# Optimization experiments

Hardware: AMD Instinct MI355X
Metric: run time of the kernel (lower is better)

## Reference

```python
import jax, jax.numpy as jnp
import numpy as np

N = 100000      # nodes
E = 3200000     # edges (avg degree 32)
IN, HID, OUT = 512, 256, 64
K = 10
ALPHA = 0.1


def setup_inputs() -> dict:
    key = jax.random.key(0)
    k1, k2, k3, k4 = jax.random.split(key, 4)
    x = jax.random.normal(k1, (N, IN), dtype=jnp.float32)
    edge_index = jax.random.randint(k2, (2, E), 0, N, dtype=jnp.int64)
    # MLP params (Kaiming-ish scaling)
    W1 = jax.random.normal(k3, (IN, HID), dtype=jnp.float32) / np.sqrt(IN)
    b1 = jnp.zeros((HID,), dtype=jnp.float32)
    W2 = jax.random.normal(k4, (HID, OUT), dtype=jnp.float32) / np.sqrt(HID)
    b2 = jnp.zeros((OUT,), dtype=jnp.float32)
    # GPR_prop PPR init: temp[k] = alpha*(1-alpha)^k, temp[K] = (1-alpha)^K
    ks = np.arange(K + 1)
    temp = ALPHA * (1.0 - ALPHA) ** ks
    temp[-1] = (1.0 - ALPHA) ** K
    temp = jnp.asarray(temp, dtype=jnp.float32)
    return {"x": x, "edge_index": edge_index, "W1": W1, "b1": b1,
            "W2": W2, "b2": b2, "temp": temp}


def reference(x, edge_index, W1, b1, W2, b2, temp):
    # MLP front-end (eval mode: dropout = identity)
    h = jax.nn.relu(x @ W1 + b1)
    h = h @ W2 + b2                                  # [N, OUT]

    # gcn_norm with self-loops: A_hat = D^{-1/2} (A + I) D^{-1/2}
    loop = jnp.arange(N, dtype=edge_index.dtype)
    src = jnp.concatenate([edge_index[0], loop])      # [E+N]
    dst = jnp.concatenate([edge_index[1], loop])      # [E+N]
    deg = jax.ops.segment_sum(jnp.ones_like(dst, dtype=h.dtype), dst,
                              num_segments=N)
    dis = jnp.where(deg > 0, jax.lax.rsqrt(deg), 0.0)
    norm = (dis[src] * dis[dst])[:, None]             # [E+N, 1]

    # GPR propagation: out = sum_k temp[k] * A_hat^k h
    def step(carry, gamma):
        hk, acc = carry
        hk = jax.ops.segment_sum(norm * hk[src], dst, num_segments=N)
        return (hk, acc + gamma * hk), None

    (_, out), _ = jax.lax.scan(step, (h, temp[0] * h), temp[1:])
    return out
```

## Files before the change

### kernel.cpp

```cpp
#include <hip/hip_runtime.h>

#define NN 100000
#define NE 3200000
#define DIN 512
#define DHID 256
#define DOUT 64
#define KPROP 10
#define NPART 8
#define PSZ 12500

typedef _Float16 f16;
typedef _Float16 f16x8 __attribute__((ext_vector_type(8)));
typedef _Float16 f16x4 __attribute__((ext_vector_type(4)));
typedef float f32x4 __attribute__((ext_vector_type(4)));

__global__ void detect_i64(const int* __restrict__ ei, int* __restrict__ flag) {
  int lane = threadIdx.x;
  int ok = 1;
  for (int i = lane; i < 512; i += 64)
    if (ei[2 * i + 1] != 0) ok = 0;
  ok = __all(ok);
  if (lane == 0) *flag = ok;
}

__global__ void zero_cnt(int* __restrict__ cnt) {
  int g = blockIdx.x * blockDim.x + threadIdx.x;
  if (g < NN) cnt[g] = 0;
}

__global__ __launch_bounds__(256) void count_deg(
    const int* __restrict__ ei, const int* __restrict__ flag,
    int* __restrict__ cnt) {
  int p = blockIdx.x & 7;
  int chunk = blockIdx.x >> 3;
  int e0 = chunk * 1024 + threadIdx.x * 4;
  if (e0 >= NE) return;
  int is64 = *flag;
  int d0, d1, d2, d3;
  if (is64) {
    int4 a = *(const int4*)&ei[2 * (size_t)NE + 2 * (size_t)e0];
    int4 b = *(const int4*)&ei[2 * (size_t)NE + 2 * (size_t)e0 + 4];
    d0 = a.x; d1 = a.z; d2 = b.x; d3 = b.z;
  } else {
    int4 a = *(const int4*)&ei[(size_t)NE + e0];
    d0 = a.x; d1 = a.y; d2 = a.z; d3 = a.w;
  }
  int lo = p * PSZ, hi = lo + PSZ;
  if (d0 >= lo && d0 < hi) atomicAdd(&cnt[d0], 1);
  if (d1 >= lo && d1 < hi) atomicAdd(&cnt[d1], 1);
  if (d2 >= lo && d2 < hi) atomicAdd(&cnt[d2], 1);
  if (d3 >= lo && d3 < hi) atomicAdd(&cnt[d3], 1);
}

__global__ void scan1(const int* __restrict__ cnt, int* __restrict__ rs,
                      int* __restrict__ bsum) {
  __shared__ int tmp[1024];
  int t = threadIdx.x;
  int g = blockIdx.x * 1024 + t;
  int v = (g < NN) ? cnt[g] : 0;
  tmp[t] = v;
  __syncthreads();
  for (int off = 1; off < 1024; off <<= 1) {
    int y = (t >= off) ? tmp[t - off] : 0;
    __syncthreads();
    tmp[t] += y;
    __syncthreads();
  }
  if (g < NN) rs[g] = tmp[t] - v;
  if (t == 1023) bsum[blockIdx.x] = tmp[t];
}

__global__ void scan2(int* __restrict__ bsum, int nb) {
  if (blockIdx.x == 0 && threadIdx.x == 0) {
    int s = 0;
    for (int i = 0; i < nb; i++) { int v = bsum[i]; bsum[i] = s; s += v; }
  }
}

__global__ void scan3_and_dis(int* __restrict__ rs, const int* __restrict__ bsum,
                              int* __restrict__ cursor, const int* __restrict__ cnt,
                              float* __restrict__ dis) {
  int g = blockIdx.x * blockDim.x + threadIdx.x;
  if (g < NN) {
    int v = rs[g] + bsum[g >> 10];
    rs[g] = v;
    cursor[g] = v;
    dis[g] = rsqrtf((float)(cnt[g] + 1));
  }
}

__global__ __launch_bounds__(256) void fill_csr(
    const int* __restrict__ ei, const int* __restrict__ flag,
    const float* __restrict__ dis, int* __restrict__ cursor,
    int2* __restrict__ recs) {
  int p = blockIdx.x & 7;
  int chunk = blockIdx.x >> 3;
  int e0 = chunk * 1024 + threadIdx.x * 4;
  if (e0 >= NE) return;
  int is64 = *flag;
  int d[4];
  if (is64) {
    int4 a = *(const int4*)&ei[2 * (size_t)NE + 2 * (size_t)e0];
    int4 b = *(const int4*)&ei[2 * (size_t)NE + 2 * (size_t)e0 + 4];
    d[0] = a.x; d[1] = a.z; d[2] = b.x; d[3] = b.z;
  } else {
    int4 a = *(const int4*)&ei[(size_t)NE + e0];
    d[0] = a.x; d[1] = a.y; d[2] = a.z; d[3] = a.w;
  }
  int lo = p * PSZ, hi = lo + PSZ;
  #pragma unroll
  for (int j = 0; j < 4; j++) {
    if (d[j] >= lo && d[j] < hi) {
      int s = is64 ? ei[2 * (size_t)(e0 + j)] : ei[e0 + j];
      int pos = atomicAdd(&cursor[d[j]], 1);
      recs[pos] = make_int2(s, __float_as_int(dis[s] * dis[d[j]]));
    }
  }
}

__global__ void cvt_weights(const float* __restrict__ W1, const float* __restrict__ W2,
                            f16* __restrict__ W1t, f16* __restrict__ W2t) {
  int g = blockIdx.x * 256 + threadIdx.x;
  if (g < DIN * DHID) {
    int k = g >> 8, n = g & 255;
    W1t[(size_t)n * DIN + k] = (f16)W1[g];
  }
  if (g < DHID * DOUT) {
    int k = g >> 6, n = g & 63;
    W2t[(size_t)n * DHID + k] = (f16)W2[g];
  }
}

__global__ __launch_bounds__(256) void mlp_mfma(
    const float* __restrict__ x, const f16* __restrict__ W1t,
    const float* __restrict__ b1, const f16* __restrict__ W2t,
    const float* __restrict__ b2, const float* __restrict__ temp,
    f16* __restrict__ h, f16* __restrict__ z)
{
  __shared__ __align__(16) char smraw[2 * 64 * 136 * 2];
  f16* xsb = (f16*)smraw;
  f16* h1s = (f16*)smraw;
  int t = threadIdx.x;
  int lane = t & 63;
  int w = t >> 6;
  int n0 = blockIdx.x * 64;
  int r15 = lane & 15;
  int g4 = lane >> 4;
  int nbase = w * 64;
  int srow = t >> 5, sc4 = t & 31;

  f32x4 acc[4][4];
  #pragma unroll
  for (int nt = 0; nt < 4; nt++) {
    float bv = b1[nbase + nt * 16 + r15];
    #pragma unroll
    for (int mt = 0; mt < 4; mt++) acc[mt][nt] = (f32x4){bv, bv, bv, bv};
  }

  float4 ld[8];
  #pragma unroll
  for (int it = 0; it < 8; it++) {
    int row = srow + it * 8;
    int gr = n0 + row;
    ld[it] = (gr < NN) ? *(const float4*)&x[(size_t)gr * DIN + sc4 * 4]
                       : make_float4(0.f, 0.f, 0.f, 0.f);
  }
  #pragma unroll
  for (int it = 0; it < 8; it++) {
    int row = srow + it * 8;
    f16x4 hv = { (f16)ld[it].x, (f16)ld[it].y, (f16)ld[it].z, (f16)ld[it].w };
    *(f16x4*)&xsb[row * 136 + sc4 * 4] = hv;
  }
  __syncthreads();

  for (int c = 0; c < 4; c++) {
    int cur = c & 1;
    if (c < 3) {
      #pragma unroll
      for (int it = 0; it < 8; it++) {
        int row = srow + it * 8;
        int gr = n0 + row;
        ld[it] = (gr < NN)
            ? *(const float4*)&x[(size_t)gr * DIN + (c + 1) * 128 + sc4 * 4]
            : make_float4(0.f, 0.f, 0.f, 0.f);
      }
    }
    int k0 = c * 128;
    const f16* xs = xsb + cur * 8704;
    #pragma unroll
    for (int ks = 0; ks < 4; ks++) {
      int kk = ks * 32 + g4 * 8;
      f16x8 a[4], b[4];
      #pragma unroll
      for (int mt = 0; mt < 4; mt++)
        a[mt] = *(const f16x8*)&xs[(mt * 16 + r15) * 136 + kk];
      #pragma unroll
      for (int nt = 0; nt < 4; nt++)
        b[nt] = *(const f16x8*)&W1t[(size_t)(nbase + nt * 16 + r15) * DIN + k0 + kk];
      #pragma unroll
      for (int mt = 0; mt < 4; mt++)
        #pragma unroll
        for (int nt = 0; nt < 4; nt++)
          acc[mt][nt] = __builtin_amdgcn_mfma_f32_16x16x32_f16(a[mt], b[nt], acc[mt][nt], 0, 0, 0);
    }
    if (c < 3) {
      #pragma unroll
      for (int it = 0; it < 8; it++) {
        int row = srow + it * 8;
        f16x4 hv = { (f16)ld[it].x, (f16)ld[it].y, (f16)ld[it].z, (f16)ld[it].w };
        *(f16x4*)&xsb[(cur ^ 1) * 8704 + row * 136 + sc4 * 4] = hv;
      }
    }
    __syncthreads();
  }

  #pragma unroll
  for (int mt = 0; mt < 4; mt++)
    #pragma unroll
    for (int nt = 0; nt < 4; nt++)
      #pragma unroll
      for (int r = 0; r < 4; r++) {
        float v = fmaxf(acc[mt][nt][r], 0.f);
        h1s[(mt * 16 + g4 * 4 + r) * 264 + nbase + nt * 16 + r15] = (f16)v;
      }
  __syncthreads();

  f32x4 acc2[4];
  #pragma unroll
  for (int nt = 0; nt < 4; nt++) {
    float bv = b2[nt * 16 + r15];
    acc2[nt] = (f32x4){bv, bv, bv, bv};
  }
  #pragma unroll
  for (int ks = 0; ks < 8; ks++) {
    int kk = ks * 32 + g4 * 8;
    f16x8 a2 = *(const f16x8*)&h1s[(w * 16 + r15) * 264 + kk];
    #pragma unroll
    for (int nt = 0; nt < 4; nt++) {
      f16x8 bf = *(const f16x8*)&W2t[(size_t)(nt * 16 + r15) * DHID + kk];
      acc2[nt] = __builtin_amdgcn_mfma_f32_16x16x32_f16(a2, bf, acc2[nt], 0, 0, 0);
    }
  }
  float tK = temp[KPROP];
  #pragma unroll
  for (int nt = 0; nt < 4; nt++)
    #pragma unroll
    for (int r = 0; r < 4; r++) {
      int node = n0 + w * 16 + g4 * 4 + r;
      if (node < NN) {
        int colv = nt * 16 + r15;
        float v = acc2[nt][r];
        h[(size_t)node * DOUT + colv] = (f16)v;
        z[(size_t)node * DOUT + colv] = (f16)(tK * v);
      }
    }
}

__global__ __launch_bounds__(256) void prop_horner(
    const f16* __restrict__ z, f16* __restrict__ zn, const f16* __restrict__ h,
    float* __restrict__ out, const int* __restrict__ rs, const int* __restrict__ cnt,
    const int2* __restrict__ recs, const float* __restrict__ dis,
    const float* __restrict__ temp, int kidx, int final_step)
{
  int w = blockIdx.x * 4 + (threadIdx.x >> 6);
  int lane = threadIdx.x & 63;
  if (w >= NN) return;
  int q = lane >> 3;
  int s8 = lane & 7;

  float acc[8];
  #pragma unroll
  for (int f = 0; f < 8; f++) acc[f] = 0.f;

  int beg = rs[w], n = cnt[w];
  const int2* rp = recs + beg;

  int e = 0;
  for (; e + 32 <= n; e += 32) {
    int2 r0 = rp[e + q];
    int2 r1 = rp[e + 8 + q];
    int2 r2 = rp[e + 16 + q];
    int2 r3 = rp[e + 24 + q];
    f16x8 g0 = *(const f16x8*)&z[(size_t)r0.x * DOUT + s8 * 8];
    f16x8 g1 = *(const f16x8*)&z[(size_t)r1.x * DOUT + s8 * 8];
    f16x8 g2 = *(const f16x8*)&z[(size_t)r2.x * DOUT + s8 * 8];
    f16x8 g3 = *(const f16x8*)&z[(size_t)r3.x * DOUT + s8 * 8];
    float w0 = __int_as_float(r0.y);
    float w1 = __int_as_float(r1.y);
    float w2 = __int_as_float(r2.y);
    float w3 = __int_as_float(r3.y);
    #pragma unroll
    for (int f = 0; f < 8; f++) acc[f] = fmaf(w0, (float)g0[f], acc[f]);
    #pragma unroll
    for (int f = 0; f < 8; f++) acc[f] = fmaf(w1, (float)g1[f], acc[f]);
    #pragma unroll
    for (int f = 0; f < 8; f++) acc[f] = fmaf(w2, (float)g2[f], acc[f]);
    #pragma unroll
    for (int f = 0; f < 8; f++) acc[f] = fmaf(w3, (float)g3[f], acc[f]);
  }
  for (; e + 8 <= n; e += 8) {
    int2 r0 = rp[e + q];
    f16x8 g0 = *(const f16x8*)&z[(size_t)r0.x * DOUT + s8 * 8];
    float w0 = __int_as_float(r0.y);
    #pragma unroll
    for (int f = 0; f < 8; f++) acc[f] = fmaf(w0, (float)g0[f], acc[f]);
  }
  if (e < n) {
    int rem = n - e;
    int qq = q < rem ? q : rem - 1;
    int2 r0 = rp[e + qq];
    f16x8 g0 = *(const f16x8*)&z[(size_t)r0.x * DOUT + s8 * 8];
    float w0 = (q < rem) ? __int_as_float(r0.y) : 0.f;
    #pragma unroll
    for (int f = 0; f < 8; f++) acc[f] = fmaf(w0, (float)g0[f], acc[f]);
  }

  #pragma unroll
  for (int f = 0; f < 8; f++) {
    acc[f] += __shfl_xor(acc[f], 8);
    acc[f] += __shfl_xor(acc[f], 16);
    acc[f] += __shfl_xor(acc[f], 32);
  }

  if (q == 0) {
    float dd = dis[w];
    float dd2 = dd * dd;
    float gk = temp[kidx];
    f16x8 zs = *(const f16x8*)&z[(size_t)w * DOUT + s8 * 8];
    f16x8 hs = *(const f16x8*)&h[(size_t)w * DOUT + s8 * 8];
    #pragma unroll
    for (int f = 0; f < 8; f++)
      acc[f] += dd2 * (float)zs[f] + gk * (float)hs[f];
    if (final_step) {
      float4 o0 = { acc[0], acc[1], acc[2], acc[3] };
      float4 o1 = { acc[4], acc[5], acc[6], acc[7] };
      *(float4*)&out[(size_t)w * DOUT + s8 * 8] = o0;
      *(float4*)&out[(size_t)w * DOUT + s8 * 8 + 4] = o1;
    } else {
      f16x8 o;
      #pragma unroll
      for (int f = 0; f < 8; f++) o[f] = (f16)acc[f];
      *(f16x8*)&zn[(size_t)w * DOUT + s8 * 8] = o;
    }
  }
}

extern "C" void kernel_launch(void* const* d_in, const int* in_sizes, int n_in,
                              void* d_out, int out_size, void* d_ws, size_t ws_size,
                              hipStream_t stream) {
  const float* x    = (const float*)d_in[0];
  const int*   ei   = (const int*)d_in[1];
  const float* W1   = (const float*)d_in[2];
  const float* b1   = (const float*)d_in[3];
  const float* W2   = (const float*)d_in[4];
  const float* b2   = (const float*)d_in[5];
  const float* temp = (const float*)d_in[6];
  float* out = (float*)d_out;

  char* wsb = (char*)d_ws;
  size_t off = 0;
  auto carve = [&](size_t bytes) -> void* {
    void* p = wsb + off;
    off = (off + bytes + 255) & ~(size_t)255;
    return p;
  };
  int*   cnt    = (int*)carve((size_t)NN * 4);
  int*   rs     = (int*)carve((size_t)NN * 4);
  int*   cursor = (int*)carve((size_t)NN * 4);
  int*   bsum   = (int*)carve(128 * 4);
  int*   flag   = (int*)carve(256);
  float* dis    = (float*)carve((size_t)NN * 4);
  int2*  recs   = (int2*)carve((size_t)NE * 8);
  f16*   W1t    = (f16*)carve((size_t)DHID * DIN * 2);
  f16*   W2t    = (f16*)carve((size_t)DOUT * DHID * 2);
  f16*   h_buf  = (f16*)carve((size_t)NN * DOUT * 2);
  f16*   z_a    = (f16*)carve((size_t)NN * DOUT * 2);
  f16*   z_b    = (f16*)carve((size_t)NN * DOUT * 2);
  if (off > ws_size) return;

  int nchunks = NE / 1024;

  detect_i64<<<1, 64, 0, stream>>>(ei, flag);
  zero_cnt<<<(NN + 255) / 256, 256, 0, stream>>>(cnt);
  count_deg<<<nchunks * NPART, 256, 0, stream>>>(ei, flag, cnt);
  scan1<<<(NN + 1023) / 1024, 1024, 0, stream>>>(cnt, rs, bsum);
  scan2<<<1, 64, 0, stream>>>(bsum, (NN + 1023) / 1024);
  scan3_and_dis<<<(NN + 255) / 256, 256, 0, stream>>>(rs, bsum, cursor, cnt, dis);
  fill_csr<<<nchunks * NPART, 256, 0, stream>>>(ei, flag, dis, cursor, recs);

  cvt_weights<<<(DIN * DHID + 255) / 256, 256, 0, stream>>>(W1, W2, W1t, W2t);
  mlp_mfma<<<(NN + 63) / 64, 256, 0, stream>>>(x, W1t, b1, W2t, b2, temp, h_buf, z_a);

  const f16* zc = z_a;
  f16* zn = z_b;
  for (int k = KPROP - 1; k >= 0; k--) {
    prop_horner<<<(NN + 3) / 4, 256, 0, stream>>>(zc, zn, h_buf, out, rs, cnt,
                                                  recs, dis, temp, k, k == 0);
    const f16* t2 = zn;
    zn = (f16*)zc;
    zc = t2;
  }
}
```

Measured before the change: 1.017 ms.

## Store features in 16-column blocks and propagate per feature block

The MLP now writes h and z in a column-blocked layout (four blocks of 16 features, each holding all nodes contiguously). Propagation launches separate block groups per feature block, with two threads per destination node each gathering 16 bytes. Each pass over a feature block only touches a 3.2 MB slice of z, which is meant to stay cache-resident and improve gather locality. In exchange, the edge records are read four times, each thread walks its edge list serially with no cross-lane reduction, and the 32-byte gathers per node are narrower than the previous 128-byte rows.

```diff
diff --git a/kernel.cpp b/kernel.cpp
--- a/kernel.cpp
+++ b/kernel.cpp
@@ -8,6 +8,7 @@
 #define KPROP 10
 #define NPART 8
 #define PSZ 12500
+#define NBLK 782
 
 typedef _Float16 f16;
 typedef _Float16 f16x8 __attribute__((ext_vector_type(8)));
@@ -135,7 +136,7 @@
     const float* __restrict__ x, const f16* __restrict__ W1t,
     const float* __restrict__ b1, const f16* __restrict__ W2t,
     const float* __restrict__ b2, const float* __restrict__ temp,
-    f16* __restrict__ h, f16* __restrict__ z)
+    f16* __restrict__ hcm, f16* __restrict__ zcm)
 {
   __shared__ __align__(16) char smraw[2 * 64 * 136 * 2];
   f16* xsb = (f16*)smraw;
@@ -248,100 +249,80 @@
     for (int r = 0; r < 4; r++) {
       int node = n0 + w * 16 + g4 * 4 + r;
       if (node < NN) {
-        int colv = nt * 16 + r15;
+        size_t o = (size_t)nt * NN * 16 + (size_t)node * 16 + r15;
         float v = acc2[nt][r];
-        h[(size_t)node * DOUT + colv] = (f16)v;
-        z[(size_t)node * DOUT + colv] = (f16)(tK * v);
+        hcm[o] = (f16)v;
+        zcm[o] = (f16)(tK * v);
       }
     }
 }
 
-__global__ __launch_bounds__(256) void prop_horner(
-    const f16* __restrict__ z, f16* __restrict__ zn, const f16* __restrict__ h,
+__global__ __launch_bounds__(256) void prop_fb(
+    const f16* __restrict__ z, f16* __restrict__ zn, const f16* __restrict__ hcm,
     float* __restrict__ out, const int* __restrict__ rs, const int* __restrict__ cnt,
     const int2* __restrict__ recs, const float* __restrict__ dis,
     const float* __restrict__ temp, int kidx, int final_step)
 {
-  int w = blockIdx.x * 4 + (threadIdx.x >> 6);
-  int lane = threadIdx.x & 63;
-  if (w >= NN) return;
-  int q = lane >> 3;
-  int s8 = lane & 7;
+  int fb = blockIdx.x / NBLK;
+  int nb = blockIdx.x - fb * NBLK;
+  int t = threadIdx.x;
+  int dst = nb * 128 + (t >> 1);
+  if (dst >= NN) return;
+  int p = t & 1;
+  const f16* zs = z + (size_t)fb * NN * 16 + p * 8;
 
   float acc[8];
   #pragma unroll
   for (int f = 0; f < 8; f++) acc[f] = 0.f;
 
-  int beg = rs[w], n = cnt[w];
+  int beg = rs[dst], n = cnt[dst];
   const int2* rp = recs + beg;
-
   int e = 0;
-  for (; e + 32 <= n; e += 32) {
-    int2 r0 = rp[e + q];
-    int2 r1 = rp[e + 8 + q];
-    int2 r2 = rp[e + 16 + q];
-    int2 r3 = rp[e + 24 + q];
-    f16x8 g0 = *(const f16x8*)&z[(size_t)r0.x * DOUT + s8 * 8];
-    f16x8 g1 = *(const f16x8*)&z[(size_t)r1.x * DOUT + s8 * 8];
-    f16x8 g2 = *(const f16x8*)&z[(size_t)r2.x * DOUT + s8 * 8];
-    f16x8 g3 = *(const f16x8*)&z[(size_t)r3.x * DOUT + s8 * 8];
+  for (; e + 4 <= n; e += 4) {
+    int2 r0 = rp[e + 0], r1 = rp[e + 1], r2 = rp[e + 2], r3 = rp[e + 3];
+    f16x8 g0 = *(const f16x8*)&zs[(size_t)r0.x * 16];
+    f16x8 g1 = *(const f16x8*)&zs[(size_t)r1.x * 16];
+    f16x8 g2 = *(const f16x8*)&zs[(size_t)r2.x * 16];
+    f16x8 g3 = *(const f16x8*)&zs[(size_t)r3.x * 16];
+    float w0 = __int_as_float(r0.y), w1 = __int_as_float(r1.y);
+    float w2 = __int_as_float(r2.y), w3 = __int_as_float(r3.y);
+    #pragma unroll
+    for (int f = 0; f < 8; f++) acc[f] = fmaf(w0, (float)g0[f], acc[f]);
+    #pragma unroll
+    for (int f = 0; f < 8; f++) acc[f] = fmaf(w1, (float)g1[f], acc[f]);
+    #pragma unroll
+    for (int f = 0; f < 8; f++) acc[f] = fmaf(w2, (float)g2[f], acc[f]);
+    #pragma unroll
+    for (int f = 0; f < 8; f++) acc[f] = fmaf(w3, (float)g3[f], acc[f]);
+  }
+  for (; e < n; ++e) {
+    int2 r0 = rp[e];
+    f16x8 g0 = *(const f16x8*)&zs[(size_t)r0.x * 16];
     float w0 = __int_as_float(r0.y);
-    float w1 = __int_as_float(r1.y);
-    float w2 = __int_as_float(r2.y);
-    float w3 = __int_as_float(r3.y);
     #pragma unroll
     for (int f = 0; f < 8; f++) acc[f] = fmaf(w0, (float)g0[f], acc[f]);
-    #pragma unroll
-    for (int f = 0; f < 8; f++) acc[f] = fmaf(w1, (float)g1[f], acc[f]);
-    #pragma unroll
-    for (int f = 0; f < 8; f++) acc[f] = fmaf(w2, (float)g2[f], acc[f]);
-    #pragma unroll
-    for (int f = 0; f < 8; f++) acc[f] = fmaf(w3, (float)g3[f], acc[f]);
-  }
-  for (; e + 8 <= n; e += 8) {
-    int2 r0 = rp[e + q];
-    f16x8 g0 = *(const f16x8*)&z[(size_t)r0.x * DOUT + s8 * 8];
-    float w0 = __int_as_float(r0.y);
-    #pragma unroll
-    for (int f = 0; f < 8; f++) acc[f] = fmaf(w0, (float)g0[f], acc[f]);
-  }
-  if (e < n) {
-    int rem = n - e;
-    int qq = q < rem ? q : rem - 1;
-    int2 r0 = rp[e + qq];
-    f16x8 g0 = *(const f16x8*)&z[(size_t)r0.x * DOUT + s8 * 8];
-    float w0 = (q < rem) ? __int_as_float(r0.y) : 0.f;
-    #pragma unroll
-    for (int f = 0; f < 8; f++) acc[f] = fmaf(w0, (float)g0[f], acc[f]);
-  }
-
-  #pragma unroll
-  for (int f = 0; f < 8; f++) {
-    acc[f] += __shfl_xor(acc[f], 8);
-    acc[f] += __shfl_xor(acc[f], 16);
-    acc[f] += __shfl_xor(acc[f], 32);
-  }
-
-  if (q == 0) {
-    float dd = dis[w];
-    float dd2 = dd * dd;
-    float gk = temp[kidx];
-    f16x8 zs = *(const f16x8*)&z[(size_t)w * DOUT + s8 * 8];
-    f16x8 hs = *(const f16x8*)&h[(size_t)w * DOUT + s8 * 8];
-    #pragma unroll
-    for (int f = 0; f < 8; f++)
-      acc[f] += dd2 * (float)zs[f] + gk * (float)hs[f];
-    if (final_step) {
-      float4 o0 = { acc[0], acc[1], acc[2], acc[3] };
-      float4 o1 = { acc[4], acc[5], acc[6], acc[7] };
-      *(float4*)&out[(size_t)w * DOUT + s8 * 8] = o0;
-      *(float4*)&out[(size_t)w * DOUT + s8 * 8 + 4] = o1;
-    } else {
-      f16x8 o;
-      #pragma unroll
-      for (int f = 0; f < 8; f++) o[f] = (f16)acc[f];
-      *(f16x8*)&zn[(size_t)w * DOUT + s8 * 8] = o;
-    }
+  }
+
+  float dd = dis[dst];
+  float dd2 = dd * dd;
+  float gk = temp[kidx];
+  f16x8 zf = *(const f16x8*)&zs[(size_t)dst * 16];
+  f16x8 hf = *(const f16x8*)&hcm[(size_t)fb * NN * 16 + (size_t)dst * 16 + p * 8];
+  #pragma unroll
+  for (int f = 0; f < 8; f++)
+    acc[f] += dd2 * (float)zf[f] + gk * (float)hf[f];
+
+  if (final_step) {
+    float4 o0 = { acc[0], acc[1], acc[2], acc[3] };
+    float4 o1 = { acc[4], acc[5], acc[6], acc[7] };
+    size_t o = (size_t)dst * DOUT + fb * 16 + p * 8;
+    *(float4*)&out[o] = o0;
+    *(float4*)&out[o + 4] = o1;
+  } else {
+    f16x8 ov;
+    #pragma unroll
+    for (int f = 0; f < 8; f++) ov[f] = (f16)acc[f];
+    *(f16x8*)&zn[(size_t)fb * NN * 16 + (size_t)dst * 16 + p * 8] = ov;
   }
 }
 
@@ -373,7 +354,7 @@
   int2*  recs   = (int2*)carve((size_t)NE * 8);
   f16*   W1t    = (f16*)carve((size_t)DHID * DIN * 2);
   f16*   W2t    = (f16*)carve((size_t)DOUT * DHID * 2);
-  f16*   h_buf  = (f16*)carve((size_t)NN * DOUT * 2);
+  f16*   h_cm   = (f16*)carve((size_t)NN * DOUT * 2);
   f16*   z_a    = (f16*)carve((size_t)NN * DOUT * 2);
   f16*   z_b    = (f16*)carve((size_t)NN * DOUT * 2);
   if (off > ws_size) return;
@@ -389,13 +370,13 @@
   fill_csr<<<nchunks * NPART, 256, 0, stream>>>(ei, flag, dis, cursor, recs);
 
   cvt_weights<<<(DIN * DHID + 255) / 256, 256, 0, stream>>>(W1, W2, W1t, W2t);
-  mlp_mfma<<<(NN + 63) / 64, 256, 0, stream>>>(x, W1t, b1, W2t, b2, temp, h_buf, z_a);
+  mlp_mfma<<<(NN + 63) / 64, 256, 0, stream>>>(x, W1t, b1, W2t, b2, temp, h_cm, z_a);
 
   const f16* zc = z_a;
   f16* zn = z_b;
   for (int k = KPROP - 1; k >= 0; k--) {
-    prop_horner<<<(NN + 3) / 4, 256, 0, stream>>>(zc, zn, h_buf, out, rs, cnt,
-                                                  recs, dis, temp, k, k == 0);
+    prop_fb<<<NBLK * 4, 256, 0, stream>>>(zc, zn, h_cm, out, rs, cnt, recs,
+                                          dis, temp, k, k == 0);
     const f16* t2 = zn;
     zn = (f16*)zc;
     zc = t2;
```

After: 2.001 ms. 96.7% more time.
